# Kernel optimization log

Measured on AMD Instinct MI355X. Metric: run time of the kernel, lower is better.

The kernel has to match this reference:

```python
import jax, jax.numpy as jnp
import numpy as np

N = 8192
IN_CH = 256
OUT_CH = 64
LEAKY_ALPHA = 0.5
NEG_INF = -9e15  # -9000000000000000.0 from the source


def setup_inputs() -> dict:
    key = jax.random.key(0)
    k1, k2, k3, k4 = jax.random.split(key, 4)
    h = jax.random.normal(k1, (N, IN_CH), dtype=jnp.float32)
    adj = jax.random.randint(k2, (N, N), 0, 2, dtype=jnp.int32)
    # Xavier-uniform-style init for parameters
    limW = float(np.sqrt(6.0 / (IN_CH + OUT_CH)))
    W = jax.random.uniform(k3, (IN_CH, OUT_CH), dtype=jnp.float32, minval=-limW, maxval=limW)
    lima = float(np.sqrt(6.0 / (2 * OUT_CH + 1)))
    a = jax.random.uniform(k4, (2 * OUT_CH, 1), dtype=jnp.float32, minval=-lima, maxval=lima)
    return {"h": h, "adj": adj, "W": W, "a": a}


def reference(h, adj, W, a):
    # Wh: [N, out]
    Wh = h @ W
    # additive attention score: e[i,j] = leakyrelu(Wh[i]@a1 + Wh[j]@a2)
    Wh1 = Wh @ a[:OUT_CH]   # [N, 1]
    Wh2 = Wh @ a[OUT_CH:]   # [N, 1]
    e = Wh1 + Wh2.T         # [N, N]
    e = jnp.where(e >= 0, e, LEAKY_ALPHA * e)  # LeakyReLU(0.5)
    # adjacency masking + row softmax
    att = jnp.where(adj > 0, e, jnp.float32(NEG_INF))
    att = jax.nn.softmax(att, axis=1)
    # dropout is identity in eval mode (training=False)
    h_prime = att @ Wh      # [N, out]
    # concat=True branch applies ReLU on the output
    return jax.nn.relu(h_prime)
```

## Files before the change

### kernel.cpp

```cpp
#include <hip/hip_runtime.h>
#include <stdint.h>

#define NN 8192
#define INC 256
#define OUTC 64
#define LOG2E 1.4426950408889634f

typedef __bf16 bf16x8 __attribute__((ext_vector_type(8)));
typedef float f32x4 __attribute__((ext_vector_type(4)));

__device__ __forceinline__ unsigned short f2bf(float x) {
    union { float f; unsigned u; } v; v.f = x;
    unsigned u = v.u;
    u += 0x7fffu + ((u >> 16) & 1u);
    return (unsigned short)(u >> 16);
}

#if __has_builtin(__builtin_amdgcn_exp2f)
#define EXP2(x) __builtin_amdgcn_exp2f(x)
#else
#define EXP2(x) exp2f(x)
#endif

__global__ __launch_bounds__(256) void gat_k1(
        const float* __restrict__ h, const float* __restrict__ W,
        const float* __restrict__ a,
        unsigned short* __restrict__ WhTf, float* __restrict__ Wh1,
        float* __restrict__ Wh2) {
    __shared__ float Ws[256 * 65];
    __shared__ float hs[16 * INC];
    __shared__ float Wa1s[256], Wa2s[256], as_[128];
    __shared__ unsigned short wt[OUTC][16];
    const int r0 = blockIdx.x * 16;
    const int t  = threadIdx.x;
    if (t < 128) as_[t] = a[t];
    #pragma unroll
    for (int it = 0; it < 16; ++it) {
        int idx = it * 1024 + t * 4;
        float4 v = *reinterpret_cast<const float4*>(W + idx);
        int k = idx >> 6, c = idx & 63;
        float* dst = &Ws[k * 65 + c];
        dst[0] = v.x; dst[1] = v.y; dst[2] = v.z; dst[3] = v.w;
    }
    #pragma unroll
    for (int it = 0; it < 4; ++it) {
        int idx = it * 1024 + t * 4;
        float4 v = *reinterpret_cast<const float4*>(h + (size_t)r0 * INC + idx);
        hs[idx] = v.x; hs[idx + 1] = v.y; hs[idx + 2] = v.z; hs[idx + 3] = v.w;
    }
    __syncthreads();
    {
        float s1 = 0.f, s2 = 0.f;
        #pragma unroll 8
        for (int c = 0; c < OUTC; ++c) {
            float w = Ws[t * 65 + c];
            s1 = fmaf(w, as_[c], s1);
            s2 = fmaf(w, as_[OUTC + c], s2);
        }
        Wa1s[t] = s1; Wa2s[t] = s2;
    }
    __syncthreads();
    const int w = t >> 6, lane = t & 63;
    const int c = lane;
    const float* hr = &hs[w * 4 * INC];
    float acc0 = 0.f, acc1 = 0.f, acc2 = 0.f, acc3 = 0.f;
    #pragma unroll 8
    for (int k = 0; k < INC; ++k) {
        float wv = Ws[k * 65 + c];
        acc0 = fmaf(hr[k],           wv, acc0);
        acc1 = fmaf(hr[INC + k],     wv, acc1);
        acc2 = fmaf(hr[2 * INC + k], wv, acc2);
        acc3 = fmaf(hr[3 * INC + k], wv, acc3);
    }
    float s1r[4] = {0.f, 0.f, 0.f, 0.f}, s2r[4] = {0.f, 0.f, 0.f, 0.f};
    #pragma unroll
    for (int kk = 0; kk < 4; ++kk) {
        int k = kk * 64 + lane;
        float wa1v = Wa1s[k], wa2v = Wa2s[k];
        #pragma unroll
        for (int r = 0; r < 4; ++r) {
            float hv = hr[r * INC + k];
            s1r[r] = fmaf(hv, wa1v, s1r[r]);
            s2r[r] = fmaf(hv, wa2v, s2r[r]);
        }
    }
    #pragma unroll
    for (int r = 0; r < 4; ++r) {
        float s1 = s1r[r], s2 = s2r[r];
        #pragma unroll
        for (int off = 32; off; off >>= 1) {
            s1 += __shfl_xor(s1, off, 64);
            s2 += __shfl_xor(s2, off, 64);
        }
        if (lane == 0) { Wh1[r0 + w * 4 + r] = s1; Wh2[r0 + w * 4 + r] = s2; }
    }
    wt[c][w * 4 + 0] = f2bf(acc0);
    wt[c][w * 4 + 1] = f2bf(acc1);
    wt[c][w * 4 + 2] = f2bf(acc2);
    wt[c][w * 4 + 3] = f2bf(acc3);
    __syncthreads();
    if (t < 128) {
        int m = t & 15, ct = (t >> 4) & 3, oct = t >> 6;
        int Kb = r0 >> 5;
        int qh = (r0 >> 3) & 3;
        int lanef = (qh + oct) * 16 + m;
        int cidx = ct * 16 + m;
        ushort4 v0, v1;
        v0.x = wt[cidx][oct * 8 + 0]; v0.y = wt[cidx][oct * 8 + 1];
        v0.z = wt[cidx][oct * 8 + 2]; v0.w = wt[cidx][oct * 8 + 3];
        v1.x = wt[cidx][oct * 8 + 4]; v1.y = wt[cidx][oct * 8 + 5];
        v1.z = wt[cidx][oct * 8 + 6]; v1.w = wt[cidx][oct * 8 + 7];
        unsigned short* dst = WhTf + (((size_t)(Kb * 4 + ct)) << 9) + lanef * 8;
        *reinterpret_cast<ushort4*>(dst)     = v0;
        *reinterpret_cast<ushort4*>(dst + 4) = v1;
    }
}

__global__ void gat_k2(const float* __restrict__ Wh2, float* __restrict__ M) {
    __shared__ float red[16];
    int t = threadIdx.x;
    float4 v0 = *reinterpret_cast<const float4*>(Wh2 + t * 4);
    float4 v1 = *reinterpret_cast<const float4*>(Wh2 + 4096 + t * 4);
    float m = fmaxf(fmaxf(fmaxf(v0.x, v0.y), fmaxf(v0.z, v0.w)),
                    fmaxf(fmaxf(v1.x, v1.y), fmaxf(v1.z, v1.w)));
    #pragma unroll
    for (int off = 32; off; off >>= 1) m = fmaxf(m, __shfl_xor(m, off, 64));
    if ((t & 63) == 0) red[t >> 6] = m;
    __syncthreads();
    if (t == 0) {
        float mm = red[0];
        #pragma unroll
        for (int i = 1; i < 16; ++i) mm = fmaxf(mm, red[i]);
        *M = mm;
    }
}

__global__ __launch_bounds__(256, 5) void gat_k3(
        const int* __restrict__ adj, const unsigned short* __restrict__ WhTf,
        const float* __restrict__ Wh1, const float* __restrict__ Wh2,
        const float* __restrict__ Mp, float* __restrict__ out) {
    __shared__ float accs[4][16 * OUTC];
    __shared__ float ls[4][16];
    const int r0 = blockIdx.x * 16;
    const int t = threadIdx.x;
    const int w = t >> 6, lane = t & 63;
    const int m = lane & 15, q = lane >> 4;
    const int qo = q * 8;
    const int row = r0 + m;
    const float wh1 = Wh1[row];
    const float Mv = *Mp;
    const float sM = wh1 + Mv;
    const float mhat = fmaxf(sM, 0.5f * sM);
    const float mh2 = mhat * LOG2E;
    const int* __restrict__ arow = adj + (size_t)row * NN;
    f32x4 acc[4] = {{0,0,0,0},{0,0,0,0},{0,0,0,0},{0,0,0,0}};
    float lpart = 0.f;

    int4 c0 = *reinterpret_cast<const int4*>(arow + (size_t)w * 32 + qo);
    int4 c1 = *reinterpret_cast<const int4*>(arow + (size_t)w * 32 + qo + 4);
    int4 d0 = *reinterpret_cast<const int4*>(arow + (size_t)(w + 4) * 32 + qo);
    int4 d1 = *reinterpret_cast<const int4*>(arow + (size_t)(w + 4) * 32 + qo + 4);

    #pragma unroll 2
    for (int i = 0; i < 64; ++i) {
        const int jt = w + i * 4;
        const unsigned short* fb = WhTf + (size_t)jt * 2048 + lane * 8;
        bf16x8 bv0 = *reinterpret_cast<const bf16x8*>(fb);
        bf16x8 bv1 = *reinterpret_cast<const bf16x8*>(fb + 512);
        bf16x8 bv2 = *reinterpret_cast<const bf16x8*>(fb + 1024);
        bf16x8 bv3 = *reinterpret_cast<const bf16x8*>(fb + 1536);
        const int jb = jt * 32 + qo;
        float4 s0 = *reinterpret_cast<const float4*>(Wh2 + jb);
        float4 s1 = *reinterpret_cast<const float4*>(Wh2 + jb + 4);
        const int jn = (i < 62) ? (jt + 8) : w;
        const int* __restrict__ an = arow + (size_t)jn * 32 + qo;
        int4 e0 = *reinterpret_cast<const int4*>(an);
        int4 e1 = *reinterpret_cast<const int4*>(an + 4);
        float sv[8] = {s0.x, s0.y, s0.z, s0.w, s1.x, s1.y, s1.z, s1.w};
        int   av[8] = {c0.x, c0.y, c0.z, c0.w, c1.x, c1.y, c1.z, c1.w};
        float p[8];
        #pragma unroll
        for (int e = 0; e < 8; ++e) {
            float s  = wh1 + sv[e];
            float lk = fmaxf(s, 0.5f * s);
            float ar = fmaf(lk, LOG2E, -mh2);
            float pe = EXP2(ar);
            p[e] = (av[e] > 0) ? pe : 0.f;
        }
        lpart += ((p[0] + p[1]) + (p[2] + p[3])) + ((p[4] + p[5]) + (p[6] + p[7]));
        bf16x8 af;
        #pragma unroll
        for (int e = 0; e < 8; ++e) af[e] = (__bf16)p[e];
        acc[0] = __builtin_amdgcn_mfma_f32_16x16x32_bf16(af, bv0, acc[0], 0, 0, 0);
        acc[1] = __builtin_amdgcn_mfma_f32_16x16x32_bf16(af, bv1, acc[1], 0, 0, 0);
        acc[2] = __builtin_amdgcn_mfma_f32_16x16x32_bf16(af, bv2, acc[2], 0, 0, 0);
        acc[3] = __builtin_amdgcn_mfma_f32_16x16x32_bf16(af, bv3, acc[3], 0, 0, 0);
        c0 = d0; c1 = d1; d0 = e0; d1 = e1;
    }
    #pragma unroll
    for (int ct = 0; ct < 4; ++ct)
        #pragma unroll
        for (int r = 0; r < 4; ++r)
            accs[w][(q * 4 + r) * OUTC + ct * 16 + m] = acc[ct][r];
    float l = lpart;
    l += __shfl_xor(l, 16, 64);
    l += __shfl_xor(l, 32, 64);
    if (lane < 16) ls[w][lane] = l;
    __syncthreads();
    #pragma unroll
    for (int e = t; e < 16 * OUTC; e += 256) {
        int rr = e >> 6, cc = e & 63;
        float s = (accs[0][e] + accs[1][e]) + (accs[2][e] + accs[3][e]);
        float lsum = (ls[0][rr] + ls[1][rr]) + (ls[2][rr] + ls[3][rr]);
        float o = s / lsum;
        out[(size_t)(r0 + rr) * OUTC + cc] = o > 0.f ? o : 0.f;
    }
}

extern "C" void kernel_launch(void* const* d_in, const int* in_sizes, int n_in,
                              void* d_out, int out_size, void* d_ws, size_t ws_size,
                              hipStream_t stream) {
    const float* h   = (const float*)d_in[0];
    const int*   adj = (const int*)d_in[1];
    const float* W   = (const float*)d_in[2];
    const float* a   = (const float*)d_in[3];
    float* out = (float*)d_out;

    char* base = (char*)d_ws;
    float* Wh1 = (float*)(base);
    float* Wh2 = (float*)(base + 32768);
    float* Mp  = (float*)(base + 65536);
    unsigned short* WhTf = (unsigned short*)(base + 69632);

    gat_k1<<<NN / 16, 256, 0, stream>>>(h, W, a, WhTf, Wh1, Wh2);
    gat_k2<<<1, 1024, 0, stream>>>(Wh2, Mp);
    gat_k3<<<NN / 16, 256, 0, stream>>>(adj, WhTf, Wh1, Wh2, Mp, out);
}
```

Before: 481.0 us.

## Split attention column range across blocks with a separate reduction kernel

The main attention kernel now splits the 8192 neighbour columns into four chunks along a second grid dimension. Each block writes partial numerators and softmax denominators to workspace, and a new kernel sums the chunks, normalises and applies ReLU. Occupancy hint raised from 5 to 8 blocks per CU. This is meant to expose more blocks and memory parallelism for streaming the large adjacency matrix, at the cost of extra partial-sum traffic and one more launch.

```diff
diff --git a/kernel.cpp b/kernel.cpp
--- a/kernel.cpp
+++ b/kernel.cpp
@@ -5,6 +5,7 @@
 #define INC 256
 #define OUTC 64
 #define LOG2E 1.4426950408889634f
+#define JSPLIT 4
 
 typedef __bf16 bf16x8 __attribute__((ext_vector_type(8)));
 typedef float f32x4 __attribute__((ext_vector_type(4)));
@@ -135,13 +136,16 @@
     }
 }
 
-__global__ __launch_bounds__(256, 5) void gat_k3(
+__global__ __launch_bounds__(256, 8) void gat_k3(
         const int* __restrict__ adj, const unsigned short* __restrict__ WhTf,
         const float* __restrict__ Wh1, const float* __restrict__ Wh2,
-        const float* __restrict__ Mp, float* __restrict__ out) {
+        const float* __restrict__ Mp, float* __restrict__ pacc,
+        float* __restrict__ pl) {
     __shared__ float accs[4][16 * OUTC];
     __shared__ float ls[4][16];
     const int r0 = blockIdx.x * 16;
+    const int split = blockIdx.y;
+    const int jbase = split * 64;
     const int t = threadIdx.x;
     const int w = t >> 6, lane = t & 63;
     const int m = lane & 15, q = lane >> 4;
@@ -156,14 +160,15 @@
     f32x4 acc[4] = {{0,0,0,0},{0,0,0,0},{0,0,0,0},{0,0,0,0}};
     float lpart = 0.f;
 
-    int4 c0 = *reinterpret_cast<const int4*>(arow + (size_t)w * 32 + qo);
-    int4 c1 = *reinterpret_cast<const int4*>(arow + (size_t)w * 32 + qo + 4);
-    int4 d0 = *reinterpret_cast<const int4*>(arow + (size_t)(w + 4) * 32 + qo);
-    int4 d1 = *reinterpret_cast<const int4*>(arow + (size_t)(w + 4) * 32 + qo + 4);
+    const int jt0 = jbase + w;
+    int4 c0 = *reinterpret_cast<const int4*>(arow + (size_t)jt0 * 32 + qo);
+    int4 c1 = *reinterpret_cast<const int4*>(arow + (size_t)jt0 * 32 + qo + 4);
+    int4 d0 = *reinterpret_cast<const int4*>(arow + (size_t)(jt0 + 4) * 32 + qo);
+    int4 d1 = *reinterpret_cast<const int4*>(arow + (size_t)(jt0 + 4) * 32 + qo + 4);
 
     #pragma unroll 2
-    for (int i = 0; i < 64; ++i) {
-        const int jt = w + i * 4;
+    for (int i = 0; i < 16; ++i) {
+        const int jt = jt0 + i * 4;
         const unsigned short* fb = WhTf + (size_t)jt * 2048 + lane * 8;
         bf16x8 bv0 = *reinterpret_cast<const bf16x8*>(fb);
         bf16x8 bv1 = *reinterpret_cast<const bf16x8*>(fb + 512);
@@ -172,7 +177,7 @@
         const int jb = jt * 32 + qo;
         float4 s0 = *reinterpret_cast<const float4*>(Wh2 + jb);
         float4 s1 = *reinterpret_cast<const float4*>(Wh2 + jb + 4);
-        const int jn = (i < 62) ? (jt + 8) : w;
+        const int jn = (i < 14) ? (jt + 8) : jt0;
         const int* __restrict__ an = arow + (size_t)jn * 32 + qo;
         int4 e0 = *reinterpret_cast<const int4*>(an);
         int4 e1 = *reinterpret_cast<const int4*>(an + 4);
@@ -207,14 +212,38 @@
     l += __shfl_xor(l, 32, 64);
     if (lane < 16) ls[w][lane] = l;
     __syncthreads();
+    float* pa = pacc + ((size_t)split * NN + r0) * OUTC;
     #pragma unroll
     for (int e = t; e < 16 * OUTC; e += 256) {
         int rr = e >> 6, cc = e & 63;
         float s = (accs[0][e] + accs[1][e]) + (accs[2][e] + accs[3][e]);
-        float lsum = (ls[0][rr] + ls[1][rr]) + (ls[2][rr] + ls[3][rr]);
-        float o = s / lsum;
-        out[(size_t)(r0 + rr) * OUTC + cc] = o > 0.f ? o : 0.f;
-    }
+        pa[e] = s;
+        if (cc == 0) pl[(size_t)split * NN + r0 + rr] =
+            (ls[0][rr] + ls[1][rr]) + (ls[2][rr] + ls[3][rr]);
+    }
+}
+
+__global__ __launch_bounds__(256) void gat_k4(
+        const float* __restrict__ pacc, const float* __restrict__ pl,
+        float* __restrict__ out) {
+    const int idx4 = (blockIdx.x * 256 + threadIdx.x) * 4;
+    const int row = idx4 >> 6;
+    f32x4 s = {0.f, 0.f, 0.f, 0.f};
+    float l = 0.f;
+    #pragma unroll
+    for (int sp = 0; sp < JSPLIT; ++sp) {
+        f32x4 v = *reinterpret_cast<const f32x4*>(pacc + (size_t)sp * NN * OUTC + idx4);
+        s += v;
+        l += pl[(size_t)sp * NN + row];
+    }
+    float rl = 1.0f / l;
+    f32x4 o;
+    #pragma unroll
+    for (int e = 0; e < 4; ++e) {
+        float v = s[e] * rl;
+        o[e] = v > 0.f ? v : 0.f;
+    }
+    *reinterpret_cast<f32x4*>(out + idx4) = o;
 }
 
 extern "C" void kernel_launch(void* const* d_in, const int* in_sizes, int n_in,
@@ -231,8 +260,11 @@
     float* Wh2 = (float*)(base + 32768);
     float* Mp  = (float*)(base + 65536);
     unsigned short* WhTf = (unsigned short*)(base + 69632);
+    float* pacc = (float*)(base + 2166784);
+    float* pl   = (float*)(base + 2166784 + (size_t)JSPLIT * NN * OUTC * 4);
 
     gat_k1<<<NN / 16, 256, 0, stream>>>(h, W, a, WhTf, Wh1, Wh2);
     gat_k2<<<1, 1024, 0, stream>>>(Wh2, Mp);
-    gat_k3<<<NN / 16, 256, 0, stream>>>(adj, WhTf, Wh1, Wh2, Mp, out);
-}
+    gat_k3<<<dim3(NN / 16, JSPLIT), 256, 0, stream>>>(adj, WhTf, Wh1, Wh2, Mp, pacc, pl);
+    gat_k4<<<NN * OUTC / 1024, 256, 0, stream>>>(pacc, pl, out);
+}
```

New measurement: 426.4 us. -11.4%, faster.
